# Performance work log

Hardware: AMD Instinct MI355X
Metric: run time of the kernel (lower is better)

The kernel has to match this reference:

```python
import jax, jax.numpy as jnp
import numpy as np
import math

NUM_SEGMENTS = 4      # num_bezier_segments
SHARPNESS = 75.0
SAMPLE_RATE = 16      # curve samples per bezier segment


def _control_radians(S):
    # replicates the __init__ control-polygon angle construction
    theta = math.pi * 2 / (4 * S) + math.atan(math.tan(2 * math.pi / (4 * S)) / 3.0)
    r = []
    for i in range(S):
        base = 2 * math.pi / S * i
        r += [base, base + theta, 2 * math.pi / S * (i + 1) - theta]
    return jnp.asarray(np.asarray(r, dtype=np.float32).reshape(S, 3))


def _quat_rotate_inv(q, p):
    # rotate p (...,3) by the conjugate of quaternion q (...,4), wxyz convention
    q = q / jnp.linalg.norm(q, axis=-1, keepdims=True)
    w = q[..., 0:1]
    v = -q[..., 1:4]
    t = 2.0 * jnp.cross(v, p)
    return p + w * t + jnp.cross(v, t)


def _csg_stump(points, primitive_parameters, iw, uw, is_training):
    pp = jnp.swapaxes(primitive_parameters, 1, 2)          # (B,K,P)
    B, K, P = pp.shape
    S, R = NUM_SEGMENTS, SAMPLE_RATE
    quat = pp[:, :, :4]
    trans = pp[:, :, 4:7]
    height = pp[:, :, 7]                                   # (B,K)
    radius = jnp.abs(pp[:, :, 8:8 + 3 * S].reshape(B, K, S, 3))
    wts = jnp.abs(pp[:, :, 8 + 3 * S:8 + 5 * S].reshape(B, K, S, 2))

    rad = _control_radians(S)                              # (S,3)
    cp = jnp.stack([jnp.cos(rad) * radius, jnp.sin(rad) * radius], axis=-1)  # (B,K,S,3,2)

    # closed rational cubic bezier spline: segment s uses cp[s,0..2] and cp[s+1,0]
    P0, P1, P2 = cp[:, :, :, 0], cp[:, :, :, 1], cp[:, :, :, 2]
    P3 = jnp.roll(P0, -1, axis=2)
    t = jnp.arange(R, dtype=pp.dtype) / R                  # (R,) endpoint-free
    b0 = (1 - t) ** 3; b1 = 3 * t * (1 - t) ** 2; b2 = 3 * t ** 2 * (1 - t); b3 = t ** 3
    w1 = wts[..., 0:1]; w2 = wts[..., 1:2]                 # (B,K,S,1)
    num = (b0[:, None] * P0[..., None, :]
           + (b1[:, None] * w1[..., None]) * P1[..., None, :]
           + (b2[:, None] * w2[..., None]) * P2[..., None, :]
           + b3[:, None] * P3[..., None, :])               # (B,K,S,R,2)
    den = b0 + b1 * w1 + b2 * w2 + b3                       # (B,K,S,R)
    curve = (num / den[..., None]).reshape(B, K, S * R, 2)  # (B,K,N,2)

    # transform query points into each primitive's local frame
    p_loc = _quat_rotate_inv(quat[:, None], points[:, :, None, :] - trans[:, None])  # (B,M,K,3)
    pxy = p_loc[..., :2]
    pz = p_loc[..., 2]

    # point-to-curve distances without materializing the (B,M,K,N,2) diff
    p_sq = jnp.sum(pxy * pxy, axis=-1)                      # (B,M,K)
    c_sq = jnp.sum(curve * curve, axis=-1)                  # (B,K,N)
    dots = jnp.einsum('bmkd,bknd->bmkn', pxy, curve)
    d = jnp.sqrt(jnp.maximum(p_sq[..., None] + c_sq[:, None] - 2.0 * dots, 0.0) + 1e-12)
    ud = jnp.min(d, axis=-1)                                # (B,M,K) unsigned 2D distance
    idx = jnp.argmin(d, axis=-1)
    curve_r = jnp.sqrt(c_sq)                                # (B,K,N)
    r_near = jnp.take_along_axis(jnp.broadcast_to(curve_r[:, None], d.shape),
                                 idx[..., None], axis=-1)[..., 0]
    sign = jax.lax.stop_gradient(jnp.where(jnp.sqrt(p_sq) <= r_near, -1.0, 1.0))
    sdf2d = sign * ud

    # extrusion along z
    dz = jnp.abs(pz) - height[:, None, :]
    primitive_sdf = (jnp.minimum(jnp.maximum(sdf2d, dz), 0.0)
                     + jnp.sqrt(jnp.maximum(sdf2d, 0.0) ** 2 + jnp.maximum(dz, 0.0) ** 2 + 1e-12))
    support_distances = ud

    occ = jax.nn.sigmoid(-primitive_sdf * SHARPNESS)        # (B,M,K)

    # soft intersection: bkc,bmk->bmkc selection
    pre_i = iw[:, None] * occ[..., None] + (1.0 - iw)[:, None]    # (B,M,K,C)
    if is_training:
        w = jax.lax.stop_gradient(jax.nn.softmax(pre_i * -40.0, axis=-2))
        inter = jnp.sum(w * pre_i, axis=-2)                 # (B,M,C)
    else:
        inter = jnp.min(pre_i, axis=-2)

    # soft union
    pre_u = uw[:, None, :] * inter                          # (B,M,C)
    if is_training:
        w = jax.lax.stop_gradient(jax.nn.softmax(pre_u * 40.0, axis=-1))
        occupancies = jnp.sum(w * pre_u, axis=-1)           # (B,M)
    else:
        occupancies = jnp.max(pre_u, axis=-1)

    return occupancies, primitive_sdf, inter, support_distances


def setup_inputs() -> dict:
    key = jax.random.key(0)
    k1, k2, k3, k4 = jax.random.split(key, 4)
    B, M, K, C = 4, 8192, 64, 32
    P = 8 + 5 * NUM_SEGMENTS  # 28
    return {
        'sample_point_coordinates': jax.random.uniform(k1, (B, M, 3), dtype=jnp.float32),
        'primitive_parameters': jax.random.normal(k2, (B, P, K), dtype=jnp.float32),
        'intersection_layer_weights': jax.random.uniform(k3, (B, K, C), dtype=jnp.float32),
        'union_layer_weights': jax.random.uniform(k4, (B, C), dtype=jnp.float32),
        'is_training': 1,
    }


def reference(sample_point_coordinates, primitive_parameters, intersection_layer_weights,
              union_layer_weights, is_training):
    return _csg_stump(sample_point_coordinates, primitive_parameters,
                      intersection_layer_weights, union_layer_weights, bool(is_training))
```

## Files before the change

kernel.cpp:

```cpp
#include <hip/hip_runtime.h>
#include <math.h>

#define Bb 4
#define Mm 8192
#define Kk 64
#define Cc 32
#define Nn 64
#define Pp 28

#define OFF_PSDF  (Bb*Mm)
#define OFF_INTER (Bb*Mm + Bb*Mm*Kk)
#define OFF_SD    (Bb*Mm + Bb*Mm*Kk + Bb*Mm*Cc)

#define W40    57.707801635558535f
#define NL2_40 (-0.017328679513998632f)
#define S75    108.20212806667225f

struct Rad12 { float v[12]; };

__device__ __forceinline__ float fexp2(float x){ return __builtin_amdgcn_exp2f(x); }
__device__ __forceinline__ float frcp(float x){ return __builtin_amdgcn_rcpf(x); }
__device__ __forceinline__ float bperm(int idx4, float v){
    return __int_as_float(__builtin_amdgcn_ds_bpermute(idx4, __float_as_int(v)));
}

__global__ __launch_bounds__(256)
void curve_prep(const float* __restrict__ pp, Rad12 rad,
                float2* __restrict__ m2c_ws, float2* __restrict__ csqp_ws,
                float* __restrict__ params_ws)
{
    const int g = blockIdx.x * 256 + threadIdx.x;
    const int k = g & 63;
    const int n = (g >> 6) & 63;
    const int b = g >> 12;

#define PP(p) pp[((b * Pp) + (p)) * Kk + k]

    const int s  = n >> 4;
    const int it = n & 15;
    const float t = (float)it * 0.0625f;
    const int s1 = (s + 1) & 3;

    float r0 = fabsf(PP(8 + 3 * s + 0));
    float r1 = fabsf(PP(8 + 3 * s + 1));
    float r2 = fabsf(PP(8 + 3 * s + 2));
    float r3 = fabsf(PP(8 + 3 * s1 + 0));
    float w1 = fabsf(PP(20 + 2 * s + 0));
    float w2 = fabsf(PP(20 + 2 * s + 1));

    float a0 = rad.v[3 * s + 0], a1 = rad.v[3 * s + 1];
    float a2 = rad.v[3 * s + 2], a3 = rad.v[3 * s1 + 0];

    float P0x = cosf(a0) * r0, P0y = sinf(a0) * r0;
    float P1x = cosf(a1) * r1, P1y = sinf(a1) * r1;
    float P2x = cosf(a2) * r2, P2y = sinf(a2) * r2;
    float P3x = cosf(a3) * r3, P3y = sinf(a3) * r3;

    float omt = 1.0f - t;
    float b0 = omt * omt * omt;
    float b1 = (3.0f * t) * (omt * omt);
    float b2 = (3.0f * (t * t)) * omt;
    float b3 = t * t * t;
    float bw1 = b1 * w1, bw2 = b2 * w2;
    float den = ((b0 + bw1) + bw2) + b3;
    float nx  = ((b0 * P0x + bw1 * P1x) + bw2 * P2x) + b3 * P3x;
    float ny  = ((b0 * P0y + bw1 * P1y) + bw2 * P2y) + b3 * P3y;

    float cx = nx / den, cy = ny / den;
    m2c_ws[(b * Nn + n) * Kk + k] = make_float2(-2.0f * cx, -2.0f * cy);
    float csq = cx * cx + cy * cy;
    ((float*)csqp_ws)[((b * (Nn/2) + (n >> 1)) * Kk + k) * 2 + (n & 1)] = csq;

    if (n < 8) {
        float val;
        if (n < 4) {
            float q0 = PP(0), q1 = PP(1), q2 = PP(2), q3 = PP(3);
            float nrm = sqrtf(q0 * q0 + q1 * q1 + q2 * q2 + q3 * q3);
            val = PP(n) / nrm;
        } else {
            val = PP(n);
        }
        params_ws[(b * Kk + k) * 8 + n] = val;
    }
#undef PP
}

__global__ __launch_bounds__(1024, 8)
void csg_main(const float* __restrict__ pts, const float* __restrict__ iw_g,
              const float* __restrict__ uw_g, const int* __restrict__ flag,
              const float2* __restrict__ m2c_ws, const float2* __restrict__ csqp_ws,
              const float* __restrict__ params_ws, float* __restrict__ out)
{
    __shared__ __align__(16) float2 s_m2c[Nn * Kk];
    __shared__ __align__(16) float2 s_csqp[(Nn/2) * Kk];
    __shared__ __align__(16) float2 s_iw[Kk * Cc];

    const int tid = threadIdx.x;
    const int bid = blockIdx.x;
    const int b   = bid >> 7;
    const int m0  = (bid & 127) << 6;

    {
        const float4* s1 = (const float4*)(m2c_ws + (size_t)b * Nn * Kk);
        float4* d1 = (float4*)s_m2c;
        d1[tid]        = s1[tid];
        d1[tid + 1024] = s1[tid + 1024];
        const float4* s2 = (const float4*)(csqp_ws + (size_t)b * (Nn/2) * Kk);
        ((float4*)s_csqp)[tid] = s2[tid];
        float w0 = iw_g[b * (Kk * Cc) + tid];
        float w1 = iw_g[b * (Kk * Cc) + tid + 1024];
        s_iw[tid]        = make_float2(w0 * (-W40), (w0 - 1.0f) * W40);
        s_iw[tid + 1024] = make_float2(w1 * (-W40), (w1 - 1.0f) * W40);
    }
    __syncthreads();

    const int wid  = tid >> 6;
    const int lane = tid & 63;
    const int pt0  = b * Mm + m0 + (wid << 2);

    const int k = lane;
    const float4* prm4 = (const float4*)(params_ws + ((b << 6) + k) * 8);
    float4 q4 = prm4[0];
    float4 t4 = prm4[1];

    const float4* pts4 = (const float4*)(pts + (size_t)pt0 * 3);
    float4 A = pts4[0], Bv = pts4[1], Cv = pts4[2];
    float pxs[4] = {A.x, A.w, Bv.z, Cv.y};
    float pys[4] = {A.y, Bv.x, Bv.w, Cv.z};
    float pzs[4] = {A.z, Bv.y, Cv.x, Cv.w};

    float plx[4], ply[4], plzv[4], psq[4];
    float vx = -q4.y, vy = -q4.z, vz = -q4.w, qw = q4.x;
#pragma unroll
    for (int p = 0; p < 4; ++p) {
        float px = pxs[p] - t4.x, py = pys[p] - t4.y, pz = pzs[p] - t4.z;
        float t1x = 2.0f * (vy * pz - vz * py);
        float t1y = 2.0f * (vz * px - vx * pz);
        float t1z = 2.0f * (vx * py - vy * px);
        plx[p]  = px + qw * t1x + (vy * t1z - vz * t1y);
        ply[p]  = py + qw * t1y + (vz * t1x - vx * t1z);
        plzv[p] = pz + qw * t1z + (vx * t1y - vy * t1x);
        psq[p]  = plx[p] * plx[p] + ply[p] * ply[p];
    }

    float bval[4] = {1e30f, 1e30f, 1e30f, 1e30f};
    float bcsq[4] = {0.0f, 0.0f, 0.0f, 0.0f};
#pragma unroll 8
    for (int n2 = 0; n2 < Nn / 2; ++n2) {
        float2 ca = s_m2c[(2 * n2) * Kk + k];
        float2 cb = s_m2c[(2 * n2 + 1) * Kk + k];
        float2 cq = s_csqp[n2 * Kk + k];
#pragma unroll
        for (int p = 0; p < 4; ++p) {
            float da = psq[p] + fmaf(ca.x, plx[p], fmaf(ca.y, ply[p], cq.x));
            if (da < bval[p]) { bval[p] = da; bcsq[p] = cq.x; }
            float db = psq[p] + fmaf(cb.x, plx[p], fmaf(cb.y, ply[p], cq.y));
            if (db < bval[p]) { bval[p] = db; bcsq[p] = cq.y; }
        }
    }

    float occ[4];
#pragma unroll
    for (int p = 0; p < 4; ++p) {
        float ud    = sqrtf(fmaxf(bval[p], 0.0f) + 1e-12f);
        float sgn   = (sqrtf(psq[p]) <= sqrtf(bcsq[p])) ? -1.0f : 1.0f;
        float sdf2d = sgn * ud;
        float dzv   = fabsf(plzv[p]) - t4.w;
        float inner = fminf(fmaxf(sdf2d, dzv), 0.0f);
        float r1m   = fmaxf(sdf2d, 0.0f), r2m = fmaxf(dzv, 0.0f);
        float psdf  = inner + sqrtf(r1m * r1m + r2m * r2m + 1e-12f);
        out[OFF_PSDF + (pt0 + p) * Kk + k] = psdf;
        out[OFF_SD   + (pt0 + p) * Kk + k] = ud;
        occ[p] = frcp(1.0f + fexp2(S75 * psdf));
    }

    const int training = flag[0];
    const int c    = lane & 31;
    const int kb   = lane & 32;
    const int idxb = kb << 2;
    const float2* iwp = s_iw + kb * Cc + c;

    float inter[4];
    if (training) {
        float sw[4]  = {0, 0, 0, 0};
        float swp[4] = {0, 0, 0, 0};
#pragma unroll
        for (int j = 0; j < 32; ++j) {
            int i4 = idxb + (j << 2);
            float2 wv = iwp[j * Cc];
#pragma unroll
            for (int p = 0; p < 4; ++p) {
                float o   = bperm(i4, occ[p]);
                float pre = fmaf(wv.x, o, wv.y);
                float e   = fexp2(pre);
                sw[p]  += e;
                swp[p]  = fmaf(e, pre, swp[p]);
            }
        }
#pragma unroll
        for (int p = 0; p < 4; ++p) {
            float swt  = sw[p]  + __shfl_xor(sw[p], 32, 64);
            float swpt = swp[p] + __shfl_xor(swp[p], 32, 64);
            inter[p] = swpt * frcp(swt) * NL2_40;
        }
    } else {
        float mx[4] = {-1e30f, -1e30f, -1e30f, -1e30f};
#pragma unroll
        for (int j = 0; j < 32; ++j) {
            int i4 = idxb + (j << 2);
            float2 wv = iwp[j * Cc];
#pragma unroll
            for (int p = 0; p < 4; ++p) {
                float o   = bperm(i4, occ[p]);
                float pre = fmaf(wv.x, o, wv.y);
                mx[p] = fmaxf(mx[p], pre);
            }
        }
#pragma unroll
        for (int p = 0; p < 4; ++p) {
            float m2 = fmaxf(mx[p], __shfl_xor(mx[p], 32, 64));
            inter[p] = m2 * NL2_40;
        }
    }

    if (lane < Cc) {
#pragma unroll
        for (int p = 0; p < 4; ++p)
            out[OFF_INTER + (pt0 + p) * Cc + c] = inter[p];
    }

    float uwv = uw_g[b * Cc + c];
    float resv[4];
    if (training) {
#pragma unroll
        for (int p = 0; p < 4; ++p) {
            float pu  = uwv * inter[p];
            float e   = fexp2(W40 * pu);
            float num = e * pu, den = e;
#pragma unroll
            for (int msk = 16; msk >= 1; msk >>= 1) {
                num += __shfl_xor(num, msk, 64);
                den += __shfl_xor(den, msk, 64);
            }
            resv[p] = num * frcp(den);
        }
    } else {
#pragma unroll
        for (int p = 0; p < 4; ++p) {
            float pu = uwv * inter[p];
#pragma unroll
            for (int msk = 16; msk >= 1; msk >>= 1)
                pu = fmaxf(pu, __shfl_xor(pu, msk, 64));
            resv[p] = pu;
        }
    }
    if (lane == 0)
        *(float4*)(out + pt0) = make_float4(resv[0], resv[1], resv[2], resv[3]);
}

extern "C" void kernel_launch(void* const* d_in, const int* in_sizes, int n_in,
                              void* d_out, int out_size, void* d_ws, size_t ws_size,
                              hipStream_t stream)
{
    const float* pts  = (const float*)d_in[0];
    const float* pp   = (const float*)d_in[1];
    const float* iw   = (const float*)d_in[2];
    const float* uw   = (const float*)d_in[3];
    const int*   flag = (const int*)d_in[4];
    float* out = (float*)d_out;

    float2* m2c_ws  = (float2*)d_ws;
    float2* csqp_ws = (float2*)((char*)d_ws + (size_t)Bb*Nn*Kk*sizeof(float2));
    float*  params_ws = (float*)((char*)d_ws + (size_t)Bb*Nn*Kk*sizeof(float2)
                                             + (size_t)Bb*(Nn/2)*Kk*sizeof(float2));

    Rad12 rad;
    const double th = M_PI * 2.0 / 16.0 + atan(tan(2.0 * M_PI / 16.0) / 3.0);
    for (int i = 0; i < 4; ++i) {
        double base = 2.0 * M_PI / 4.0 * (double)i;
        rad.v[3 * i + 0] = (float)base;
        rad.v[3 * i + 1] = (float)(base + th);
        rad.v[3 * i + 2] = (float)(2.0 * M_PI / 4.0 * (double)(i + 1) - th);
    }

    curve_prep<<<64, 256, 0, stream>>>(pp, rad, m2c_ws, csqp_ws, params_ws);
    csg_main<<<Bb * Mm / 64, 1024, 0, stream>>>(pts, iw, uw, flag,
                                                m2c_ws, csqp_ws, params_ws, out);
}
```

Measured before the change: 46.39 us.

## Use packed FMA for curve distance search and share occupancies via LDS

Curve coordinates and squared norms are now stored as separate x, y and csq planes, interleaved in pairs. The nearest-point search can then use v_pk_fma_f32 to evaluate two samples per instruction, and the constant psq term moves out of the loop. The ds_bpermute broadcasts of occupancy in the intersection stage are replaced by writing occupancies to reused LDS and reading them as float4. Shared memory is pooled into one buffer, which adds an extra __syncthreads before the curve-squared region is overwritten.

Result: faster. 45.36 us (-2.2%).

```diff
diff --git a/kernel.cpp b/kernel.cpp
--- a/kernel.cpp
+++ b/kernel.cpp
@@ -16,18 +16,22 @@
 #define NL2_40 (-0.017328679513998632f)
 #define S75    108.20212806667225f
 
+typedef float f32x2 __attribute__((ext_vector_type(2)));
+
 struct Rad12 { float v[12]; };
 
 __device__ __forceinline__ float fexp2(float x){ return __builtin_amdgcn_exp2f(x); }
 __device__ __forceinline__ float frcp(float x){ return __builtin_amdgcn_rcpf(x); }
-__device__ __forceinline__ float bperm(int idx4, float v){
-    return __int_as_float(__builtin_amdgcn_ds_bpermute(idx4, __float_as_int(v)));
+__device__ __forceinline__ f32x2 pk_fma(f32x2 a, f32x2 b, f32x2 c){
+    f32x2 d;
+    asm("v_pk_fma_f32 %0, %1, %2, %3" : "=v"(d) : "v"(a), "v"(b), "v"(c));
+    return d;
 }
 
 __global__ __launch_bounds__(256)
 void curve_prep(const float* __restrict__ pp, Rad12 rad,
-                float2* __restrict__ m2c_ws, float2* __restrict__ csqp_ws,
-                float* __restrict__ params_ws)
+                float* __restrict__ ws_cx, float* __restrict__ ws_cy,
+                float* __restrict__ ws_cq, float* __restrict__ params_ws)
 {
     const int g = blockIdx.x * 256 + threadIdx.x;
     const int k = g & 63;
@@ -67,9 +71,10 @@
     float ny  = ((b0 * P0y + bw1 * P1y) + bw2 * P2y) + b3 * P3y;
 
     float cx = nx / den, cy = ny / den;
-    m2c_ws[(b * Nn + n) * Kk + k] = make_float2(-2.0f * cx, -2.0f * cy);
-    float csq = cx * cx + cy * cy;
-    ((float*)csqp_ws)[((b * (Nn/2) + (n >> 1)) * Kk + k) * 2 + (n & 1)] = csq;
+    const int idx = ((b * 32 + (n >> 1)) * 64 + k) * 2 + (n & 1);
+    ws_cx[idx] = -2.0f * cx;
+    ws_cy[idx] = -2.0f * cy;
+    ws_cq[idx] = cx * cx + cy * cy;
 
     if (n < 8) {
         float val;
@@ -88,12 +93,11 @@
 __global__ __launch_bounds__(1024, 8)
 void csg_main(const float* __restrict__ pts, const float* __restrict__ iw_g,
               const float* __restrict__ uw_g, const int* __restrict__ flag,
-              const float2* __restrict__ m2c_ws, const float2* __restrict__ csqp_ws,
-              const float* __restrict__ params_ws, float* __restrict__ out)
+              const float* __restrict__ ws_cx, const float* __restrict__ ws_cy,
+              const float* __restrict__ ws_cq, const float* __restrict__ params_ws,
+              float* __restrict__ out)
 {
-    __shared__ __align__(16) float2 s_m2c[Nn * Kk];
-    __shared__ __align__(16) float2 s_csqp[(Nn/2) * Kk];
-    __shared__ __align__(16) float2 s_iw[Kk * Cc];
+    __shared__ __align__(16) float s_pool[16384];
 
     const int tid = threadIdx.x;
     const int bid = blockIdx.x;
@@ -101,16 +105,15 @@
     const int m0  = (bid & 127) << 6;
 
     {
-        const float4* s1 = (const float4*)(m2c_ws + (size_t)b * Nn * Kk);
-        float4* d1 = (float4*)s_m2c;
-        d1[tid]        = s1[tid];
-        d1[tid + 1024] = s1[tid + 1024];
-        const float4* s2 = (const float4*)(csqp_ws + (size_t)b * (Nn/2) * Kk);
-        ((float4*)s_csqp)[tid] = s2[tid];
-        float w0 = iw_g[b * (Kk * Cc) + tid];
-        float w1 = iw_g[b * (Kk * Cc) + tid + 1024];
-        s_iw[tid]        = make_float2(w0 * (-W40), (w0 - 1.0f) * W40);
-        s_iw[tid + 1024] = make_float2(w1 * (-W40), (w1 - 1.0f) * W40);
+        ((float4*)&s_pool[0])[tid]     = ((const float4*)(ws_cx + b * 4096))[tid];
+        ((float4*)&s_pool[4096])[tid]  = ((const float4*)(ws_cy + b * 4096))[tid];
+        ((float4*)&s_pool[8192])[tid]  = ((const float4*)(ws_cq + b * 4096))[tid];
+        float w0 = iw_g[b * 2048 + tid];
+        float w1 = iw_g[b * 2048 + tid + 1024];
+        s_pool[12288 + tid * 2]        = w0 * (-W40);
+        s_pool[12288 + tid * 2 + 1]    = (w0 - 1.0f) * W40;
+        s_pool[14336 + tid * 2]        = w1 * (-W40);
+        s_pool[14336 + tid * 2 + 1]    = (w1 - 1.0f) * W40;
     }
     __syncthreads();
 
@@ -129,7 +132,8 @@
     float pys[4] = {A.y, Bv.x, Bv.w, Cv.z};
     float pzs[4] = {A.z, Bv.y, Cv.x, Cv.w};
 
-    float plx[4], ply[4], plzv[4], psq[4];
+    f32x2 plx2[4], ply2[4];
+    float plzv[4], psq[4];
     float vx = -q4.y, vy = -q4.z, vz = -q4.w, qw = q4.x;
 #pragma unroll
     for (int p = 0; p < 4; ++p) {
@@ -137,32 +141,37 @@
         float t1x = 2.0f * (vy * pz - vz * py);
         float t1y = 2.0f * (vz * px - vx * pz);
         float t1z = 2.0f * (vx * py - vy * px);
-        plx[p]  = px + qw * t1x + (vy * t1z - vz * t1y);
-        ply[p]  = py + qw * t1y + (vz * t1x - vx * t1z);
-        plzv[p] = pz + qw * t1z + (vx * t1y - vy * t1x);
-        psq[p]  = plx[p] * plx[p] + ply[p] * ply[p];
-    }
-
-    float bval[4] = {1e30f, 1e30f, 1e30f, 1e30f};
+        float plx = px + qw * t1x + (vy * t1z - vz * t1y);
+        float ply = py + qw * t1y + (vz * t1x - vx * t1z);
+        plzv[p]   = pz + qw * t1z + (vx * t1y - vy * t1x);
+        psq[p]    = plx * plx + ply * ply;
+        plx2[p].x = plx; plx2[p].y = plx;
+        ply2[p].x = ply; ply2[p].y = ply;
+    }
+
+    float best[4] = {1e30f, 1e30f, 1e30f, 1e30f};
     float bcsq[4] = {0.0f, 0.0f, 0.0f, 0.0f};
-#pragma unroll 8
-    for (int n2 = 0; n2 < Nn / 2; ++n2) {
-        float2 ca = s_m2c[(2 * n2) * Kk + k];
-        float2 cb = s_m2c[(2 * n2 + 1) * Kk + k];
-        float2 cq = s_csqp[n2 * Kk + k];
-#pragma unroll
-        for (int p = 0; p < 4; ++p) {
-            float da = psq[p] + fmaf(ca.x, plx[p], fmaf(ca.y, ply[p], cq.x));
-            if (da < bval[p]) { bval[p] = da; bcsq[p] = cq.x; }
-            float db = psq[p] + fmaf(cb.x, plx[p], fmaf(cb.y, ply[p], cq.y));
-            if (db < bval[p]) { bval[p] = db; bcsq[p] = cq.y; }
+    const f32x2* cxp = (const f32x2*)&s_pool[k * 2];
+    const f32x2* cyp = (const f32x2*)&s_pool[4096 + k * 2];
+    const f32x2* cqp = (const f32x2*)&s_pool[8192 + k * 2];
+#pragma unroll
+    for (int j = 0; j < 32; ++j) {
+        f32x2 cx2 = cxp[j * 64];
+        f32x2 cy2 = cyp[j * 64];
+        f32x2 cq2 = cqp[j * 64];
+#pragma unroll
+        for (int p = 0; p < 4; ++p) {
+            f32x2 d = pk_fma(cx2, plx2[p], pk_fma(cy2, ply2[p], cq2));
+            if (d.x < best[p]) { best[p] = d.x; bcsq[p] = cq2.x; }
+            if (d.y < best[p]) { best[p] = d.y; bcsq[p] = cq2.y; }
         }
     }
 
     float occ[4];
 #pragma unroll
     for (int p = 0; p < 4; ++p) {
-        float ud    = sqrtf(fmaxf(bval[p], 0.0f) + 1e-12f);
+        float d2    = psq[p] + best[p];
+        float ud    = sqrtf(fmaxf(d2, 0.0f) + 1e-12f);
         float sgn   = (sqrtf(psq[p]) <= sqrtf(bcsq[p])) ? -1.0f : 1.0f;
         float sdf2d = sgn * ud;
         float dzv   = fabsf(plzv[p]) - t4.w;
@@ -174,11 +183,14 @@
         occ[p] = frcp(1.0f + fexp2(S75 * psdf));
     }
 
+    __syncthreads();
+    *(float4*)&s_pool[8192 + tid * 4] = make_float4(occ[0], occ[1], occ[2], occ[3]);
+
     const int training = flag[0];
     const int c    = lane & 31;
     const int kb   = lane & 32;
-    const int idxb = kb << 2;
-    const float2* iwp = s_iw + kb * Cc + c;
+    const float4* occp = (const float4*)&s_pool[8192 + ((wid << 6) + kb) * 4];
+    const f32x2*  iwp  = (const f32x2*)&s_pool[12288 + ((kb << 5) + c) * 2];
 
     float inter[4];
     if (training) {
@@ -186,12 +198,12 @@
         float swp[4] = {0, 0, 0, 0};
 #pragma unroll
         for (int j = 0; j < 32; ++j) {
-            int i4 = idxb + (j << 2);
-            float2 wv = iwp[j * Cc];
+            float4 o4 = occp[j];
+            f32x2 wv  = iwp[j * 32];
+            float os[4] = {o4.x, o4.y, o4.z, o4.w};
 #pragma unroll
             for (int p = 0; p < 4; ++p) {
-                float o   = bperm(i4, occ[p]);
-                float pre = fmaf(wv.x, o, wv.y);
+                float pre = fmaf(wv.x, os[p], wv.y);
                 float e   = fexp2(pre);
                 sw[p]  += e;
                 swp[p]  = fmaf(e, pre, swp[p]);
@@ -207,14 +219,12 @@
         float mx[4] = {-1e30f, -1e30f, -1e30f, -1e30f};
 #pragma unroll
         for (int j = 0; j < 32; ++j) {
-            int i4 = idxb + (j << 2);
-            float2 wv = iwp[j * Cc];
-#pragma unroll
-            for (int p = 0; p < 4; ++p) {
-                float o   = bperm(i4, occ[p]);
-                float pre = fmaf(wv.x, o, wv.y);
-                mx[p] = fmaxf(mx[p], pre);
-            }
+            float4 o4 = occp[j];
+            f32x2 wv  = iwp[j * 32];
+            float os[4] = {o4.x, o4.y, o4.z, o4.w};
+#pragma unroll
+            for (int p = 0; p < 4; ++p)
+                mx[p] = fmaxf(mx[p], fmaf(wv.x, os[p], wv.y));
         }
 #pragma unroll
         for (int p = 0; p < 4; ++p) {
@@ -269,10 +279,10 @@
     const int*   flag = (const int*)d_in[4];
     float* out = (float*)d_out;
 
-    float2* m2c_ws  = (float2*)d_ws;
-    float2* csqp_ws = (float2*)((char*)d_ws + (size_t)Bb*Nn*Kk*sizeof(float2));
-    float*  params_ws = (float*)((char*)d_ws + (size_t)Bb*Nn*Kk*sizeof(float2)
-                                             + (size_t)Bb*(Nn/2)*Kk*sizeof(float2));
+    float* ws_cx = (float*)d_ws;
+    float* ws_cy = ws_cx + 16384;
+    float* ws_cq = ws_cy + 16384;
+    float* params_ws = ws_cq + 16384;
 
     Rad12 rad;
     const double th = M_PI * 2.0 / 16.0 + atan(tan(2.0 * M_PI / 16.0) / 3.0);
@@ -283,7 +293,7 @@
         rad.v[3 * i + 2] = (float)(2.0 * M_PI / 4.0 * (double)(i + 1) - th);
     }
 
-    curve_prep<<<64, 256, 0, stream>>>(pp, rad, m2c_ws, csqp_ws, params_ws);
+    curve_prep<<<64, 256, 0, stream>>>(pp, rad, ws_cx, ws_cy, ws_cq, params_ws);
     csg_main<<<Bb * Mm / 64, 1024, 0, stream>>>(pts, iw, uw, flag,
-                                                m2c_ws, csqp_ws, params_ws, out);
-}
+                                                ws_cx, ws_cy, ws_cq, params_ws, out);
+}
```

## Skip near-zero occupancies in the intersection softmax using precomputed zero-occupancy baselines

Applied to the files above, without the earlier changes.

The training-path intersection softmax now starts from per-(batch,column) sums precomputed for zero occupancy, computed in the prep kernel. It then corrects those sums only for primitives whose occupancy exceeds a small threshold, found with a wave ballot. Occupancies move through a swizzled LDS tile instead of per-element bpermutes. Blocks shrink to 512 threads with 8 points per wave, and the curve data layout is repacked into float4 rows. This cuts the exp-heavy loop over all 64 primitives, at the cost of a tiny approximation for occupancies below the threshold and a data-dependent loop length.

Result: faster. 42.52 us (-8.3%).

```diff
diff --git a/kernel.cpp b/kernel.cpp
--- a/kernel.cpp
+++ b/kernel.cpp
@@ -5,7 +5,6 @@
 #define Mm 8192
 #define Kk 64
 #define Cc 32
-#define Nn 64
 #define Pp 28
 
 #define OFF_PSDF  (Bb*Mm)
@@ -15,19 +14,18 @@
 #define W40    57.707801635558535f
 #define NL2_40 (-0.017328679513998632f)
 #define S75    108.20212806667225f
+#define EPS_OCC 1e-6f
 
 struct Rad12 { float v[12]; };
 
 __device__ __forceinline__ float fexp2(float x){ return __builtin_amdgcn_exp2f(x); }
 __device__ __forceinline__ float frcp(float x){ return __builtin_amdgcn_rcpf(x); }
-__device__ __forceinline__ float bperm(int idx4, float v){
-    return __int_as_float(__builtin_amdgcn_ds_bpermute(idx4, __float_as_int(v)));
-}
 
 __global__ __launch_bounds__(256)
-void curve_prep(const float* __restrict__ pp, Rad12 rad,
-                float2* __restrict__ m2c_ws, float2* __restrict__ csqp_ws,
-                float* __restrict__ params_ws)
+void curve_prep(const float* __restrict__ pp, const float* __restrict__ iw_g,
+                Rad12 rad,
+                float* __restrict__ ws_c, float* __restrict__ ws_cq,
+                float* __restrict__ params_ws, float2* __restrict__ st_ws)
 {
     const int g = blockIdx.x * 256 + threadIdx.x;
     const int k = g & 63;
@@ -67,9 +65,11 @@
     float ny  = ((b0 * P0y + bw1 * P1y) + bw2 * P2y) + b3 * P3y;
 
     float cx = nx / den, cy = ny / den;
-    m2c_ws[(b * Nn + n) * Kk + k] = make_float2(-2.0f * cx, -2.0f * cy);
-    float csq = cx * cx + cy * cy;
-    ((float*)csqp_ws)[((b * (Nn/2) + (n >> 1)) * Kk + k) * 2 + (n & 1)] = csq;
+    const int j = n >> 1, h = n & 1;
+    float* base = ws_c + (((b * 32 + j) * 64) + k) * 4;
+    base[h]     = -2.0f * cx;
+    base[2 + h] = -2.0f * cy;
+    ws_cq[(((b * 32 + j) * 64) + k) * 2 + h] = cx * cx + cy * cy;
 
     if (n < 8) {
         float val;
@@ -83,17 +83,29 @@
         params_ws[(b * Kk + k) * 8 + n] = val;
     }
 #undef PP
+
+    if (blockIdx.x == 0 && threadIdx.x < 128) {
+        const int tb = threadIdx.x >> 5, tc = threadIdx.x & 31;
+        float S = 0.0f, T = 0.0f;
+        for (int kk = 0; kk < 64; ++kk) {
+            float w   = iw_g[tb * 2048 + kk * 32 + tc];
+            float b40 = (w - 1.0f) * W40;
+            float e   = fexp2(b40);
+            S += e;
+            T  = fmaf(e, b40, T);
+        }
+        st_ws[threadIdx.x] = make_float2(S, T);
+    }
 }
 
-__global__ __launch_bounds__(1024, 8)
+__global__ __launch_bounds__(512, 6)
 void csg_main(const float* __restrict__ pts, const float* __restrict__ iw_g,
               const float* __restrict__ uw_g, const int* __restrict__ flag,
-              const float2* __restrict__ m2c_ws, const float2* __restrict__ csqp_ws,
-              const float* __restrict__ params_ws, float* __restrict__ out)
+              const float* __restrict__ ws_c, const float* __restrict__ ws_cq,
+              const float* __restrict__ params_ws, const float2* __restrict__ st_ws,
+              float* __restrict__ out)
 {
-    __shared__ __align__(16) float2 s_m2c[Nn * Kk];
-    __shared__ __align__(16) float2 s_csqp[(Nn/2) * Kk];
-    __shared__ __align__(16) float2 s_iw[Kk * Cc];
+    __shared__ __align__(16) float s_pool[12352];
 
     const int tid = threadIdx.x;
     const int bid = blockIdx.x;
@@ -101,68 +113,81 @@
     const int m0  = (bid & 127) << 6;
 
     {
-        const float4* s1 = (const float4*)(m2c_ws + (size_t)b * Nn * Kk);
-        float4* d1 = (float4*)s_m2c;
-        d1[tid]        = s1[tid];
-        d1[tid + 1024] = s1[tid + 1024];
-        const float4* s2 = (const float4*)(csqp_ws + (size_t)b * (Nn/2) * Kk);
-        ((float4*)s_csqp)[tid] = s2[tid];
-        float w0 = iw_g[b * (Kk * Cc) + tid];
-        float w1 = iw_g[b * (Kk * Cc) + tid + 1024];
-        s_iw[tid]        = make_float2(w0 * (-W40), (w0 - 1.0f) * W40);
-        s_iw[tid + 1024] = make_float2(w1 * (-W40), (w1 - 1.0f) * W40);
+        const float4* cs = (const float4*)(ws_c + (size_t)b * 8192);
+        float4* cd = (float4*)s_pool;
+#pragma unroll
+        for (int i = 0; i < 4; ++i) cd[tid + i * 512] = cs[tid + i * 512];
+        const float4* qs = (const float4*)(ws_cq + (size_t)b * 4096);
+        float4* qd = (float4*)&s_pool[8192];
+#pragma unroll
+        for (int i = 0; i < 2; ++i) qd[tid + i * 512] = qs[tid + i * 512];
     }
     __syncthreads();
 
     const int wid  = tid >> 6;
     const int lane = tid & 63;
-    const int pt0  = b * Mm + m0 + (wid << 2);
-
-    const int k = lane;
+    const int k    = lane;
+    const int pt0  = b * Mm + m0 + (wid << 3);
+
     const float4* prm4 = (const float4*)(params_ws + ((b << 6) + k) * 8);
     float4 q4 = prm4[0];
     float4 t4 = prm4[1];
 
-    const float4* pts4 = (const float4*)(pts + (size_t)pt0 * 3);
-    float4 A = pts4[0], Bv = pts4[1], Cv = pts4[2];
-    float pxs[4] = {A.x, A.w, Bv.z, Cv.y};
-    float pys[4] = {A.y, Bv.x, Bv.w, Cv.z};
-    float pzs[4] = {A.z, Bv.y, Cv.x, Cv.w};
-
-    float plx[4], ply[4], plzv[4], psq[4];
-    float vx = -q4.y, vy = -q4.z, vz = -q4.w, qw = q4.x;
-#pragma unroll
-    for (int p = 0; p < 4; ++p) {
-        float px = pxs[p] - t4.x, py = pys[p] - t4.y, pz = pzs[p] - t4.z;
-        float t1x = 2.0f * (vy * pz - vz * py);
-        float t1y = 2.0f * (vz * px - vx * pz);
-        float t1z = 2.0f * (vx * py - vy * px);
-        plx[p]  = px + qw * t1x + (vy * t1z - vz * t1y);
-        ply[p]  = py + qw * t1y + (vz * t1x - vx * t1z);
-        plzv[p] = pz + qw * t1z + (vx * t1y - vy * t1x);
-        psq[p]  = plx[p] * plx[p] + ply[p] * ply[p];
-    }
-
-    float bval[4] = {1e30f, 1e30f, 1e30f, 1e30f};
-    float bcsq[4] = {0.0f, 0.0f, 0.0f, 0.0f};
+    float fl[24];
+    {
+        const float4* p4 = (const float4*)(pts + (size_t)pt0 * 3);
+#pragma unroll
+        for (int i = 0; i < 6; ++i) {
+            float4 v = p4[i];
+            fl[i * 4 + 0] = v.x; fl[i * 4 + 1] = v.y;
+            fl[i * 4 + 2] = v.z; fl[i * 4 + 3] = v.w;
+        }
+    }
+
+    float plx[8], ply[8], plzv[8], psq[8];
+    {
+        float vx = -q4.y, vy = -q4.z, vz = -q4.w, qw = q4.x;
+#pragma unroll
+        for (int p = 0; p < 8; ++p) {
+            float px = fl[3 * p + 0] - t4.x;
+            float py = fl[3 * p + 1] - t4.y;
+            float pz = fl[3 * p + 2] - t4.z;
+            float t1x = 2.0f * (vy * pz - vz * py);
+            float t1y = 2.0f * (vz * px - vx * pz);
+            float t1z = 2.0f * (vx * py - vy * px);
+            plx[p]  = px + qw * t1x + (vy * t1z - vz * t1y);
+            ply[p]  = py + qw * t1y + (vz * t1x - vx * t1z);
+            plzv[p] = pz + qw * t1z + (vx * t1y - vy * t1x);
+            psq[p]  = plx[p] * plx[p] + ply[p] * ply[p];
+        }
+    }
+
+    float best[8], bcsq[8];
+#pragma unroll
+    for (int p = 0; p < 8; ++p) { best[p] = 1e30f; bcsq[p] = 0.0f; }
+    {
+        const float4* cdp = (const float4*)&s_pool[k * 4];
+        const float2* cqp = (const float2*)&s_pool[8192 + k * 2];
 #pragma unroll 8
-    for (int n2 = 0; n2 < Nn / 2; ++n2) {
-        float2 ca = s_m2c[(2 * n2) * Kk + k];
-        float2 cb = s_m2c[(2 * n2 + 1) * Kk + k];
-        float2 cq = s_csqp[n2 * Kk + k];
-#pragma unroll
-        for (int p = 0; p < 4; ++p) {
-            float da = psq[p] + fmaf(ca.x, plx[p], fmaf(ca.y, ply[p], cq.x));
-            if (da < bval[p]) { bval[p] = da; bcsq[p] = cq.x; }
-            float db = psq[p] + fmaf(cb.x, plx[p], fmaf(cb.y, ply[p], cq.y));
-            if (db < bval[p]) { bval[p] = db; bcsq[p] = cq.y; }
-        }
-    }
-
-    float occ[4];
-#pragma unroll
-    for (int p = 0; p < 4; ++p) {
-        float ud    = sqrtf(fmaxf(bval[p], 0.0f) + 1e-12f);
+        for (int j = 0; j < 32; ++j) {
+            float4 cd  = cdp[j * 64];
+            float2 cq2 = cqp[j * 64];
+#pragma unroll
+            for (int p = 0; p < 8; ++p) {
+                float da = fmaf(cd.x, plx[p], fmaf(cd.z, ply[p], cq2.x));
+                if (da < best[p]) { best[p] = da; bcsq[p] = cq2.x; }
+                float db = fmaf(cd.y, plx[p], fmaf(cd.w, ply[p], cq2.y));
+                if (db < best[p]) { best[p] = db; bcsq[p] = cq2.y; }
+            }
+        }
+    }
+
+    float occ[8];
+    unsigned long long mask[8];
+#pragma unroll
+    for (int p = 0; p < 8; ++p) {
+        float d2    = psq[p] + best[p];
+        float ud    = sqrtf(fmaxf(d2, 0.0f) + 1e-12f);
         float sgn   = (sqrtf(psq[p]) <= sqrtf(bcsq[p])) ? -1.0f : 1.0f;
         float sdf2d = sgn * ud;
         float dzv   = fabsf(plzv[p]) - t4.w;
@@ -171,69 +196,86 @@
         float psdf  = inner + sqrtf(r1m * r1m + r2m * r2m + 1e-12f);
         out[OFF_PSDF + (pt0 + p) * Kk + k] = psdf;
         out[OFF_SD   + (pt0 + p) * Kk + k] = ud;
-        occ[p] = frcp(1.0f + fexp2(S75 * psdf));
-    }
+        occ[p]  = frcp(1.0f + fexp2(S75 * psdf));
+        mask[p] = __ballot(occ[p] > EPS_OCC);
+    }
+
+    __syncthreads();
+    {
+        const int key  = (k & 15) << 4;
+        const int colb = wid << 5;
+        char* basep = (char*)s_pool + k * 256;
+        *(float4*)(basep + ((colb)      ^ key)) = make_float4(occ[0], occ[1], occ[2], occ[3]);
+        *(float4*)(basep + ((colb + 16) ^ key)) = make_float4(occ[4], occ[5], occ[6], occ[7]);
+    }
+#pragma unroll
+    for (int i = 0; i < 4; ++i) {
+        int idx = tid + i * 512;
+        float w  = iw_g[b * 2048 + idx];
+        float a  = w * (-W40);
+        float bb = (w - 1.0f) * W40;
+        float e0 = fexp2(bb);
+        ((float2*)&s_pool[4096])[idx] = make_float2(a, bb);
+        ((float2*)&s_pool[8192])[idx] = make_float2(e0, e0 * bb);
+    }
+    if (tid < 32) ((float2*)&s_pool[12288])[tid] = st_ws[b * 32 + tid];
+    __syncthreads();
 
     const int training = flag[0];
-    const int c    = lane & 31;
-    const int kb   = lane & 32;
-    const int idxb = kb << 2;
-    const float2* iwp = s_iw + kb * Cc + c;
-
-    float inter[4];
+    const int c = lane & 31;
+    const float2* wvt = (const float2*)&s_pool[4096];
+    const float2* e0t = (const float2*)&s_pool[8192];
+
+    float inter[8];
     if (training) {
-        float sw[4]  = {0, 0, 0, 0};
-        float swp[4] = {0, 0, 0, 0};
-#pragma unroll
-        for (int j = 0; j < 32; ++j) {
-            int i4 = idxb + (j << 2);
-            float2 wv = iwp[j * Cc];
-#pragma unroll
-            for (int p = 0; p < 4; ++p) {
-                float o   = bperm(i4, occ[p]);
-                float pre = fmaf(wv.x, o, wv.y);
+        float2 s0t0 = ((const float2*)&s_pool[12288])[c];
+#pragma unroll
+        for (int p = 0; p < 8; ++p) {
+            unsigned long long m = mask[p];
+            const int pt4 = ((wid << 3) + p) << 2;
+            float sw = s0t0.x, swp = s0t0.y;
+            while (m) {
+                int kk = __builtin_ctzll(m); m &= m - 1;
+                float osv = *(const float*)((const char*)s_pool +
+                              kk * 256 + (pt4 ^ ((kk & 15) << 4)));
+                float2 wv = wvt[kk * 32 + c];
+                float2 e0 = e0t[kk * 32 + c];
+                float pre = fmaf(wv.x, osv, wv.y);
                 float e   = fexp2(pre);
-                sw[p]  += e;
-                swp[p]  = fmaf(e, pre, swp[p]);
+                sw  += (e - e0.x);
+                swp += fmaf(e, pre, -e0.y);
             }
-        }
-#pragma unroll
-        for (int p = 0; p < 4; ++p) {
-            float swt  = sw[p]  + __shfl_xor(sw[p], 32, 64);
-            float swpt = swp[p] + __shfl_xor(swp[p], 32, 64);
-            inter[p] = swpt * frcp(swt) * NL2_40;
+            inter[p] = swp * frcp(sw) * NL2_40;
         }
     } else {
-        float mx[4] = {-1e30f, -1e30f, -1e30f, -1e30f};
-#pragma unroll
-        for (int j = 0; j < 32; ++j) {
-            int i4 = idxb + (j << 2);
-            float2 wv = iwp[j * Cc];
-#pragma unroll
-            for (int p = 0; p < 4; ++p) {
-                float o   = bperm(i4, occ[p]);
-                float pre = fmaf(wv.x, o, wv.y);
-                mx[p] = fmaxf(mx[p], pre);
+        const int kb = lane & 32;
+#pragma unroll
+        for (int p = 0; p < 8; ++p) {
+            const int pt4 = ((wid << 3) + p) << 2;
+            float mx = -1e30f;
+            for (int j = 0; j < 32; ++j) {
+                int row = kb + j;
+                float osv = *(const float*)((const char*)s_pool +
+                              row * 256 + (pt4 ^ ((row & 15) << 4)));
+                float2 wv = wvt[row * 32 + c];
+                mx = fmaxf(mx, fmaf(wv.x, osv, wv.y));
             }
-        }
-#pragma unroll
-        for (int p = 0; p < 4; ++p) {
-            float m2 = fmaxf(mx[p], __shfl_xor(mx[p], 32, 64));
-            inter[p] = m2 * NL2_40;
+            mx = fmaxf(mx, __shfl_xor(mx, 32, 64));
+            inter[p] = mx * NL2_40;
         }
     }
 
     if (lane < Cc) {
 #pragma unroll
-        for (int p = 0; p < 4; ++p)
+        for (int p = 0; p < 8; ++p)
             out[OFF_INTER + (pt0 + p) * Cc + c] = inter[p];
     }
 
     float uwv = uw_g[b * Cc + c];
-    float resv[4];
+    float resv[8];
     if (training) {
 #pragma unroll
-        for (int p = 0; p < 4; ++p) {
+        for (int p = 0; p < 8; ++p) {
             float pu  = uwv * inter[p];
             float e   = fexp2(W40 * pu);
             float num = e * pu, den = e;
@@ -246,7 +288,7 @@
         }
     } else {
 #pragma unroll
-        for (int p = 0; p < 4; ++p) {
+        for (int p = 0; p < 8; ++p) {
             float pu = uwv * inter[p];
 #pragma unroll
             for (int msk = 16; msk >= 1; msk >>= 1)
@@ -254,8 +296,10 @@
             resv[p] = pu;
         }
     }
-    if (lane == 0)
-        *(float4*)(out + pt0) = make_float4(resv[0], resv[1], resv[2], resv[3]);
+    if (lane == 0) {
+        *(float4*)(out + pt0)     = make_float4(resv[0], resv[1], resv[2], resv[3]);
+        *(float4*)(out + pt0 + 4) = make_float4(resv[4], resv[5], resv[6], resv[7]);
+    }
 }
 
 extern "C" void kernel_launch(void* const* d_in, const int* in_sizes, int n_in,
@@ -269,10 +313,10 @@
     const int*   flag = (const int*)d_in[4];
     float* out = (float*)d_out;
 
-    float2* m2c_ws  = (float2*)d_ws;
-    float2* csqp_ws = (float2*)((char*)d_ws + (size_t)Bb*Nn*Kk*sizeof(float2));
-    float*  params_ws = (float*)((char*)d_ws + (size_t)Bb*Nn*Kk*sizeof(float2)
-                                             + (size_t)Bb*(Nn/2)*Kk*sizeof(float2));
+    float*  ws_c   = (float*)d_ws;
+    float*  ws_cq  = ws_c + 32768;
+    float*  params = ws_cq + 16384;
+    float2* st_ws  = (float2*)(params + 2048);
 
     Rad12 rad;
     const double th = M_PI * 2.0 / 16.0 + atan(tan(2.0 * M_PI / 16.0) / 3.0);
@@ -283,7 +327,7 @@
         rad.v[3 * i + 2] = (float)(2.0 * M_PI / 4.0 * (double)(i + 1) - th);
     }
 
-    curve_prep<<<64, 256, 0, stream>>>(pp, rad, m2c_ws, csqp_ws, params_ws);
-    csg_main<<<Bb * Mm / 64, 1024, 0, stream>>>(pts, iw, uw, flag,
-                                                m2c_ws, csqp_ws, params_ws, out);
+    curve_prep<<<64, 256, 0, stream>>>(pp, iw, rad, ws_c, ws_cq, params, st_ws);
+    csg_main<<<Bb * Mm / 64, 512, 0, stream>>>(pts, iw, uw, flag,
+                                               ws_c, ws_cq, params, st_ws, out);
 }
```
